# Performance work log

Hardware: AMD Instinct MI355X
Metric: run time of the kernel (lower is better)

The kernel has to match this reference:

```python
import jax, jax.numpy as jnp
import numpy as np

B, DEPTH, X, H, C = 512, 9, 128, 64, 16
NPT = 2 ** (DEPTH + 1) - 1  # 1023 nodes per perfect binary tree (heap layout)


def setup_inputs() -> dict:
    key = jax.random.key(0)
    ks = jax.random.split(key, 5)
    s = 0.05
    return {
        "embeddings": jax.random.normal(ks[0], (B, NPT, X), jnp.float32),
        "h0": jnp.zeros((B, NPT, H), jnp.float32),
        "c0": jnp.zeros((B, NPT, H), jnp.float32),
        "W_iou": jax.random.normal(ks[1], (X, 3 * H), jnp.float32) * s,
        "U_iou": jax.random.normal(ks[2], (2 * H, 3 * H), jnp.float32) * s,
        "b_iou": jnp.zeros((3 * H,), jnp.float32),
        "Uf_w": jax.random.normal(ks[3], (2 * H, 2 * H), jnp.float32) * s,
        "Uf_b": jnp.zeros((2 * H,), jnp.float32),
        "lin_w": jax.random.normal(ks[4], (H, C), jnp.float32) * s,
        "lin_b": jnp.zeros((C,), jnp.float32),
    }


def _apply_gates(iou, c_base):
    # apply_node_func: i,o,u chunks -> c = sig(i)*tanh(u) + c_base; h = sig(o)*tanh(c)
    i, o, u = jnp.split(iou, 3, axis=-1)
    c = jax.nn.sigmoid(i) * jnp.tanh(u) + c_base
    h = jax.nn.sigmoid(o) * jnp.tanh(c)
    return h, c


def reference(embeddings, h0, c0, W_iou, U_iou, b_iou, Uf_w, Uf_b, lin_w, lin_b):
    h, c = h0, c0
    # --- leaves (no in-edges): iou = W_iou(x) + b_iou, c_base = initial c ---
    ls = 2 ** DEPTH - 1  # first leaf index
    iou = embeddings[:, ls:] @ W_iou + b_iou
    hl, cl = _apply_gates(iou, c0[:, ls:])
    h = h.at[:, ls:].set(hl)
    c = c.at[:, ls:].set(cl)
    # --- internal levels, deepest -> root (topological propagation) ---
    for lvl in range(DEPTH - 1, -1, -1):
        s0, n = 2 ** lvl - 1, 2 ** lvl
        # children of nodes [s0, s0+n) are the contiguous block [2*s0+1, 2*s0+1+2n)
        cs = 2 * s0 + 1
        hc = h[:, cs:cs + 2 * n].reshape(B, n, 2 * H)   # h_cat = [h_left, h_right]
        cc = c[:, cs:cs + 2 * n].reshape(B, n, 2, H)
        # reduce_func: f = sigmoid(U_f(h_cat)); c_red = sum(f * c_children)
        f = jax.nn.sigmoid(hc @ Uf_w.T + Uf_b).reshape(B, n, 2, H)
        c_red = jnp.sum(f * cc, axis=2)
        # DGL overwrite semantics: internal iou = U_iou(h_cat) (+ b_iou in apply)
        iou = hc @ U_iou + b_iou
        hn, cn = _apply_gates(iou, c_red)
        h = h.at[:, s0:s0 + n].set(hn)
        c = c.at[:, s0:s0 + n].set(cn)
    # global mean pool over nodes per tree, then classifier + softmax
    hm = jnp.mean(h, axis=1)  # [B, H]
    logits = hm @ lin_w + lin_b
    return jax.nn.softmax(logits, axis=-1)
```

## Files before the change

### kernel.cpp

```cpp
#include <hip/hip_runtime.h>
#include <hip/hip_bf16.h>
#include <stdint.h>

#define NPT 1023
#define LEAF_TILES 12
#define INT_TILES  20

typedef float f32x4 __attribute__((ext_vector_type(4)));
typedef __bf16 bf16x8_t __attribute__((ext_vector_type(8)));

__device__ __forceinline__ unsigned int f32_to_bf16(float f) {
    unsigned int u = __float_as_uint(f);
    u += 0x7FFFu + ((u >> 16) & 1u);
    return u >> 16;
}
__device__ __forceinline__ float sigm(float x) {
    return __builtin_amdgcn_rcpf(1.0f + __expf(-x));
}
__device__ __forceinline__ float tanh_f(float x) {
    return 1.0f - 2.0f * __builtin_amdgcn_rcpf(1.0f + __expf(2.0f * x));
}
__device__ __forceinline__ f32x4 mfma16(uint4 a, uint4 b, f32x4 c) {
    return __builtin_amdgcn_mfma_f32_16x16x32_bf16(
        __builtin_bit_cast(bf16x8_t, a), __builtin_bit_cast(bf16x8_t, b), c, 0, 0, 0);
}

__global__ void prep_kernel(const float* __restrict__ W_iou,
                            const float* __restrict__ U_iou,
                            const float* __restrict__ Uf_w,
                            unsigned short* __restrict__ leafB,
                            unsigned short* __restrict__ intB) {
    int tid = blockIdx.x * blockDim.x + threadIdx.x;
    const int leaf_slots = LEAF_TILES * 4 * 64;
    const int total = (LEAF_TILES + INT_TILES) * 4 * 64;
    if (tid >= total) return;
    bool leaf = tid < leaf_slots;
    int s = leaf ? tid : tid - leaf_slots;
    int tile = s >> 8;
    int ks = (s >> 6) & 3;
    int l = s & 63;
    int col = tile * 16 + (l & 15);
    int k0 = ks * 32 + (l >> 4) * 8;
    unsigned short vals[8];
#pragma unroll
    for (int i = 0; i < 8; ++i) {
        int k = k0 + i;
        float v;
        if (leaf) v = W_iou[k * 192 + col];
        else      v = (col < 192) ? U_iou[k * 192 + col]
                                  : Uf_w[(col - 192) * 128 + k];
        vals[i] = (unsigned short)f32_to_bf16(v);
    }
    uint4* dst = (uint4*)(leaf ? leafB : intB);
    dst[s] = *(const uint4*)vals;
}

__global__ __launch_bounds__(256, 2) void mega_kernel(
        const float* __restrict__ emb,
        float* __restrict__ hbuf,
        float* __restrict__ cbuf,
        const unsigned short* __restrict__ leafB,
        const unsigned short* __restrict__ intB,
        const float* __restrict__ b_iou,
        const float* __restrict__ Uf_b) {
    __shared__ unsigned char cEven[32768];
    __shared__ unsigned char cOdd[16384];
    __shared__ unsigned char hB[16384];

    const int tid = threadIdx.x;
    const int t = blockIdx.x >> 2, e = blockIdx.x & 3;
    const int wave = tid >> 6, lane = tid & 63;
    const int lrow = lane & 15, kgrp = lane >> 4;
    const int c = wave * 16 + lrow;

    const uint4* BfL = (const uint4*)leafB;
    uint4 BL[12];
#pragma unroll
    for (int nt = 0; nt < 3; ++nt)
#pragma unroll
        for (int ks = 0; ks < 4; ++ks)
            BL[nt * 4 + ks] = BfL[((wave + 4 * nt) * 4 + ks) * 64 + lane];

    const float* embBase = emb + ((size_t)(t * NPT + 511 + 128 * e)) * 128;
#pragma unroll
    for (int it = 0; it < 8; ++it) {
        int qid = it * 256 + tid;
        int r = qid >> 4, j = qid & 15;
        const float* s = embBase + r * 128 + j * 8;
        float4 v0 = *(const float4*)s;
        float4 v1 = *(const float4*)(s + 4);
        uint4 pk;
        pk.x = f32_to_bf16(v0.x) | (f32_to_bf16(v0.y) << 16);
        pk.y = f32_to_bf16(v0.z) | (f32_to_bf16(v0.w) << 16);
        pk.z = f32_to_bf16(v1.x) | (f32_to_bf16(v1.y) << 16);
        pk.w = f32_to_bf16(v1.z) | (f32_to_bf16(v1.w) << 16);
        *(uint4*)&cEven[r * 256 + ((j ^ (r & 15)) << 4)] = pk;
    }
    __syncthreads();

    f32x4 acc[8][3];
#pragma unroll
    for (int mt = 0; mt < 8; ++mt)
#pragma unroll
        for (int nt = 0; nt < 3; ++nt)
            acc[mt][nt] = (f32x4){0.f, 0.f, 0.f, 0.f};
#pragma unroll
    for (int mt = 0; mt < 8; ++mt) {
        const int row = mt * 16 + lrow;
        uint4 A[4];
#pragma unroll
        for (int ks = 0; ks < 4; ++ks)
            A[ks] = *(const uint4*)&cEven[row * 256 + (((4 * ks + kgrp) ^ (row & 15)) << 4)];
#pragma unroll
        for (int nt = 0; nt < 3; ++nt)
#pragma unroll
            for (int ks = 0; ks < 4; ++ks)
                acc[mt][nt] = mfma16(A[ks], BL[nt * 4 + ks], acc[mt][nt]);
    }
    __syncthreads();

    const float bi = b_iou[c], bo = b_iou[64 + c], bu = b_iou[128 + c];
    const float bfl = Uf_b[c], bfr = Uf_b[64 + c];
    float psum = 0.f;

#pragma unroll
    for (int mt = 0; mt < 8; ++mt)
#pragma unroll
        for (int q = 0; q < 4; ++q) {
            const int row = mt * 16 + kgrp * 4 + q;
            float i_ = acc[mt][0][q] + bi;
            float o_ = acc[mt][1][q] + bo;
            float u_ = acc[mt][2][q] + bu;
            float cn = sigm(i_) * tanh_f(u_);
            float hn = sigm(o_) * tanh_f(cn);
            psum += hn;
            *(float*)&cEven[(row * 64 + c) * 4] = cn;
            *(unsigned short*)&hB[row * 128 + (((c >> 3) ^ ((row >> 1) & 7)) << 4) + (c & 7) * 2] =
                (unsigned short)f32_to_bf16(hn);
        }

    const uint4* BfI = (const uint4*)intB;
    uint4 BI[20];
#pragma unroll
    for (int nt = 0; nt < 5; ++nt)
#pragma unroll
        for (int ks = 0; ks < 4; ++ks)
            BI[nt * 4 + ks] = BfI[((wave + 4 * nt) * 4 + ks) * 64 + lane];
    __syncthreads();

    for (int lvl = 1; lvl <= 7; ++lvl) {
        const int M = 128 >> lvl;
        const int MT = (M + 15) >> 4;
        f32x4 acc2[4][5];
#pragma unroll
        for (int mt = 0; mt < 4; ++mt)
#pragma unroll
            for (int nt = 0; nt < 5; ++nt)
                acc2[mt][nt] = (f32x4){0.f, 0.f, 0.f, 0.f};
#pragma unroll
        for (int mt = 0; mt < 4; ++mt) if (mt < MT) {
            const int row = mt * 16 + lrow;
            uint4 A[4];
#pragma unroll
            for (int ks = 0; ks < 4; ++ks) {
                const int n = 2 * row + (ks >> 1);
                A[ks] = *(const uint4*)&hB[n * 128 + ((((ks & 1) * 4 + kgrp) ^ (row & 7)) << 4)];
            }
#pragma unroll
            for (int nt = 0; nt < 5; ++nt)
#pragma unroll
                for (int ks = 0; ks < 4; ++ks)
                    acc2[mt][nt] = mfma16(A[ks], BI[nt * 4 + ks], acc2[mt][nt]);
        }
        __syncthreads();
        const float* cChild = (const float*)((lvl & 1) ? cEven : cOdd);
        float* cPar = (float*)((lvl & 1) ? cOdd : cEven);
#pragma unroll
        for (int mt = 0; mt < 4; ++mt) if (mt < MT)
#pragma unroll
            for (int q = 0; q < 4; ++q) {
                const int row = mt * 16 + kgrp * 4 + q;
                if (row < M) {
                    float cl = cChild[(2 * row) * 64 + c];
                    float cr = cChild[(2 * row + 1) * 64 + c];
                    float i_ = acc2[mt][0][q] + bi;
                    float o_ = acc2[mt][1][q] + bo;
                    float u_ = acc2[mt][2][q] + bu;
                    float fl = sigm(acc2[mt][3][q] + bfl);
                    float fr = sigm(acc2[mt][4][q] + bfr);
                    float cn = sigm(i_) * tanh_f(u_) + fl * cl + fr * cr;
                    float hn = sigm(o_) * tanh_f(cn);
                    psum += hn;
                    if (lvl < 7) {
                        cPar[row * 64 + c] = cn;
                        *(unsigned short*)&hB[row * 128 + (((c >> 3) ^ ((row >> 1) & 7)) << 4) + (c & 7) * 2] =
                            (unsigned short)f32_to_bf16(hn);
                    } else {
                        size_t gi = ((size_t)(t * NPT + 3 + e)) * 64 + c;
                        hbuf[gi] = hn;
                        cbuf[gi] = cn;
                    }
                }
            }
        __syncthreads();
    }

    psum += __shfl_xor(psum, 16);
    psum += __shfl_xor(psum, 32);
    if (kgrp == 0)
        hbuf[((size_t)(t * NPT + 8 + e)) * 64 + c] = psum;
}

__global__ __launch_bounds__(256) void final_kernel(
        float* __restrict__ hbuf,
        const float* __restrict__ cbuf,
        const unsigned short* __restrict__ intB,
        const float* __restrict__ b_iou,
        const float* __restrict__ Uf_b,
        const float* __restrict__ lin_w,
        const float* __restrict__ lin_b,
        float* __restrict__ out) {
    __shared__ unsigned short hc1[16][128];
    __shared__ unsigned short hc0[16][128];
    __shared__ float sc[4][64];
    __shared__ float c12[2][64];
    __shared__ float hm[64];

    const int tid = threadIdx.x;
    const int t = blockIdx.x;
    const int wave = tid >> 6, lane = tid & 63;
    const int lrow = lane & 15, kgrp = lane >> 4;
    const int c = wave * 16 + lrow;

    {
        const int nd = tid >> 6, col = tid & 63;
        size_t gi = ((size_t)(t * NPT + 3 + nd)) * 64 + col;
        float hv = hbuf[gi];
        sc[nd][col] = cbuf[gi];
        hc1[nd >> 1][(nd & 1) * 64 + col] = (unsigned short)f32_to_bf16(hv);
    }
    const uint4* BfI = (const uint4*)intB;
    uint4 BI[20];
#pragma unroll
    for (int nt = 0; nt < 5; ++nt)
#pragma unroll
        for (int ks = 0; ks < 4; ++ks)
            BI[nt * 4 + ks] = BfI[((wave + 4 * nt) * 4 + ks) * 64 + lane];
    __syncthreads();

    const float bi = b_iou[c], bo = b_iou[64 + c], bu = b_iou[128 + c];
    const float bfl = Uf_b[c], bfr = Uf_b[64 + c];
    float psum = 0.f;

    f32x4 a1[5];
#pragma unroll
    for (int nt = 0; nt < 5; ++nt) a1[nt] = (f32x4){0.f, 0.f, 0.f, 0.f};
#pragma unroll
    for (int ks = 0; ks < 4; ++ks) {
        uint4 A = *(const uint4*)&hc1[lrow][ks * 32 + kgrp * 8];
#pragma unroll
        for (int nt = 0; nt < 5; ++nt) a1[nt] = mfma16(A, BI[nt * 4 + ks], a1[nt]);
    }
#pragma unroll
    for (int q = 0; q < 4; ++q) {
        const int row = kgrp * 4 + q;
        if (row < 2) {
            float cl = sc[2 * row][c];
            float cr = sc[2 * row + 1][c];
            float i_ = a1[0][q] + bi, o_ = a1[1][q] + bo, u_ = a1[2][q] + bu;
            float fl = sigm(a1[3][q] + bfl), fr = sigm(a1[4][q] + bfr);
            float cn = sigm(i_) * tanh_f(u_) + fl * cl + fr * cr;
            float hn = sigm(o_) * tanh_f(cn);
            psum += hn;
            c12[row][c] = cn;
            hc0[0][row * 64 + c] = (unsigned short)f32_to_bf16(hn);
        }
    }
    __syncthreads();

    f32x4 a0[5];
#pragma unroll
    for (int nt = 0; nt < 5; ++nt) a0[nt] = (f32x4){0.f, 0.f, 0.f, 0.f};
#pragma unroll
    for (int ks = 0; ks < 4; ++ks) {
        uint4 A = *(const uint4*)&hc0[lrow][ks * 32 + kgrp * 8];
#pragma unroll
        for (int nt = 0; nt < 5; ++nt) a0[nt] = mfma16(A, BI[nt * 4 + ks], a0[nt]);
    }
    if (kgrp == 0) {
        float cl = c12[0][c], cr = c12[1][c];
        float i_ = a0[0][0] + bi, o_ = a0[1][0] + bo, u_ = a0[2][0] + bu;
        float fl = sigm(a0[3][0] + bfl), fr = sigm(a0[4][0] + bfr);
        float cn = sigm(i_) * tanh_f(u_) + fl * cl + fr * cr;
        float hn = sigm(o_) * tanh_f(cn);
        psum += hn;
    }

    psum += __shfl_xor(psum, 16);
    psum += __shfl_xor(psum, 32);
    if (kgrp == 0) hm[c] = psum;
    __syncthreads();
    if (tid < 64) {
        float s = hm[tid];
#pragma unroll
        for (int e2 = 0; e2 < 4; ++e2)
            s += hbuf[((size_t)(t * NPT + 8 + e2)) * 64 + tid];
        hm[tid] = s * (1.0f / 1023.0f);
    }
    __syncthreads();
    if (tid < 16) {
        int cc = tid;
        float lg = lin_b[cc];
#pragma unroll
        for (int dd = 0; dd < 64; ++dd) lg += hm[dd] * lin_w[dd * 16 + cc];
        float mx = lg;
#pragma unroll
        for (int off = 8; off; off >>= 1) mx = fmaxf(mx, __shfl_xor(mx, off, 16));
        float ex = expf(lg - mx);
        float sm = ex;
#pragma unroll
        for (int off = 8; off; off >>= 1) sm += __shfl_xor(sm, off, 16);
        out[t * 16 + cc] = ex / sm;
    }
}

extern "C" void kernel_launch(void* const* d_in, const int* in_sizes, int n_in,
                              void* d_out, int out_size, void* d_ws, size_t ws_size,
                              hipStream_t stream) {
    const float* emb   = (const float*)d_in[0];
    float*       hbuf  = (float*)d_in[1];
    float*       cbuf  = (float*)d_in[2];
    const float* W_iou = (const float*)d_in[3];
    const float* U_iou = (const float*)d_in[4];
    const float* b_iou = (const float*)d_in[5];
    const float* Uf_w  = (const float*)d_in[6];
    const float* Uf_b  = (const float*)d_in[7];
    const float* lin_w = (const float*)d_in[8];
    const float* lin_b = (const float*)d_in[9];
    float* out = (float*)d_out;

    unsigned short* leafB = (unsigned short*)d_ws;
    unsigned short* intB  = leafB + (size_t)LEAF_TILES * 4 * 64 * 8;

    prep_kernel<<<32, 256, 0, stream>>>(W_iou, U_iou, Uf_w, leafB, intB);
    mega_kernel<<<2048, 256, 0, stream>>>(emb, hbuf, cbuf, leafB, intB, b_iou, Uf_b);
    final_kernel<<<512, 256, 0, stream>>>(hbuf, cbuf, intB, b_iou, Uf_b, lin_w, lin_b, out);
}
```

Baseline: 493.3 us.

## Cut LDS and register use to fit three blocks per CU

```diff
diff --git a/kernel.cpp b/kernel.cpp
--- a/kernel.cpp
+++ b/kernel.cpp
@@ -13,6 +13,9 @@
     unsigned int u = __float_as_uint(f);
     u += 0x7FFFu + ((u >> 16) & 1u);
     return u >> 16;
+}
+__device__ __forceinline__ float bf16_ld(const void* p) {
+    return __uint_as_float(((unsigned int)*(const unsigned short*)p) << 16);
 }
 __device__ __forceinline__ float sigm(float x) {
     return __builtin_amdgcn_rcpf(1.0f + __expf(-x));
@@ -55,7 +58,7 @@
     dst[s] = *(const uint4*)vals;
 }
 
-__global__ __launch_bounds__(256, 2) void mega_kernel(
+__global__ __launch_bounds__(256, 3) void mega_kernel(
         const float* __restrict__ emb,
         float* __restrict__ hbuf,
         float* __restrict__ cbuf,
@@ -63,9 +66,8 @@
         const unsigned short* __restrict__ intB,
         const float* __restrict__ b_iou,
         const float* __restrict__ Uf_b) {
-    __shared__ unsigned char cEven[32768];
-    __shared__ unsigned char cOdd[16384];
-    __shared__ unsigned char hB[16384];
+    __shared__ __align__(16) unsigned char cw[32768];
+    __shared__ __align__(16) unsigned char hB[16384];
 
     const int tid = threadIdx.x;
     const int t = blockIdx.x >> 2, e = blockIdx.x & 3;
@@ -94,28 +96,7 @@
         pk.y = f32_to_bf16(v0.z) | (f32_to_bf16(v0.w) << 16);
         pk.z = f32_to_bf16(v1.x) | (f32_to_bf16(v1.y) << 16);
         pk.w = f32_to_bf16(v1.z) | (f32_to_bf16(v1.w) << 16);
-        *(uint4*)&cEven[r * 256 + ((j ^ (r & 15)) << 4)] = pk;
-    }
-    __syncthreads();
-
-    f32x4 acc[8][3];
-#pragma unroll
-    for (int mt = 0; mt < 8; ++mt)
-#pragma unroll
-        for (int nt = 0; nt < 3; ++nt)
-            acc[mt][nt] = (f32x4){0.f, 0.f, 0.f, 0.f};
-#pragma unroll
-    for (int mt = 0; mt < 8; ++mt) {
-        const int row = mt * 16 + lrow;
-        uint4 A[4];
-#pragma unroll
-        for (int ks = 0; ks < 4; ++ks)
-            A[ks] = *(const uint4*)&cEven[row * 256 + (((4 * ks + kgrp) ^ (row & 15)) << 4)];
-#pragma unroll
-        for (int nt = 0; nt < 3; ++nt)
-#pragma unroll
-            for (int ks = 0; ks < 4; ++ks)
-                acc[mt][nt] = mfma16(A[ks], BL[nt * 4 + ks], acc[mt][nt]);
+        *(uint4*)&cw[r * 256 + ((j ^ (r & 15)) << 4)] = pk;
     }
     __syncthreads();
 
@@ -124,20 +105,43 @@
     float psum = 0.f;
 
 #pragma unroll
-    for (int mt = 0; mt < 8; ++mt)
-#pragma unroll
-        for (int q = 0; q < 4; ++q) {
-            const int row = mt * 16 + kgrp * 4 + q;
-            float i_ = acc[mt][0][q] + bi;
-            float o_ = acc[mt][1][q] + bo;
-            float u_ = acc[mt][2][q] + bu;
-            float cn = sigm(i_) * tanh_f(u_);
-            float hn = sigm(o_) * tanh_f(cn);
-            psum += hn;
-            *(float*)&cEven[(row * 64 + c) * 4] = cn;
-            *(unsigned short*)&hB[row * 128 + (((c >> 3) ^ ((row >> 1) & 7)) << 4) + (c & 7) * 2] =
-                (unsigned short)f32_to_bf16(hn);
+    for (int p = 0; p < 2; ++p) {
+        f32x4 acc[4][3];
+#pragma unroll
+        for (int mt = 0; mt < 4; ++mt)
+#pragma unroll
+            for (int nt = 0; nt < 3; ++nt)
+                acc[mt][nt] = (f32x4){0.f, 0.f, 0.f, 0.f};
+#pragma unroll
+        for (int mt = 0; mt < 4; ++mt) {
+            const int row = p * 64 + mt * 16 + lrow;
+            uint4 A[4];
+#pragma unroll
+            for (int ks = 0; ks < 4; ++ks)
+                A[ks] = *(const uint4*)&cw[row * 256 + (((4 * ks + kgrp) ^ (row & 15)) << 4)];
+#pragma unroll
+            for (int nt = 0; nt < 3; ++nt)
+#pragma unroll
+                for (int ks = 0; ks < 4; ++ks)
+                    acc[mt][nt] = mfma16(A[ks], BL[nt * 4 + ks], acc[mt][nt]);
         }
+        if (p == 0) __syncthreads();
+#pragma unroll
+        for (int mt = 0; mt < 4; ++mt)
+#pragma unroll
+            for (int q = 0; q < 4; ++q) {
+                const int row = p * 64 + mt * 16 + kgrp * 4 + q;
+                float i_ = acc[mt][0][q] + bi;
+                float o_ = acc[mt][1][q] + bo;
+                float u_ = acc[mt][2][q] + bu;
+                float cn = sigm(i_) * tanh_f(u_);
+                float hn = sigm(o_) * tanh_f(cn);
+                psum += hn;
+                *(unsigned short*)&cw[(row * 64 + c) * 2] = (unsigned short)f32_to_bf16(cn);
+                *(unsigned short*)&hB[row * 128 + (((c >> 3) ^ ((row >> 1) & 7)) << 4) + (c & 7) * 2] =
+                    (unsigned short)f32_to_bf16(hn);
+            }
+    }
 
     const uint4* BfI = (const uint4*)intB;
     uint4 BI[20];
@@ -148,17 +152,64 @@
             BI[nt * 4 + ks] = BfI[((wave + 4 * nt) * 4 + ks) * 64 + lane];
     __syncthreads();
 
-    for (int lvl = 1; lvl <= 7; ++lvl) {
+#pragma unroll
+    for (int p = 0; p < 2; ++p) {
+        f32x4 acc2[2][5];
+#pragma unroll
+        for (int mt = 0; mt < 2; ++mt)
+#pragma unroll
+            for (int nt = 0; nt < 5; ++nt)
+                acc2[mt][nt] = (f32x4){0.f, 0.f, 0.f, 0.f};
+#pragma unroll
+        for (int mt = 0; mt < 2; ++mt) {
+            const int row = p * 32 + mt * 16 + lrow;
+            uint4 A[4];
+#pragma unroll
+            for (int ks = 0; ks < 4; ++ks) {
+                const int n = 2 * row + (ks >> 1);
+                A[ks] = *(const uint4*)&hB[n * 128 + ((((ks & 1) * 4 + kgrp) ^ (row & 7)) << 4)];
+            }
+#pragma unroll
+            for (int nt = 0; nt < 5; ++nt)
+#pragma unroll
+                for (int ks = 0; ks < 4; ++ks)
+                    acc2[mt][nt] = mfma16(A[ks], BI[nt * 4 + ks], acc2[mt][nt]);
+        }
+        if (p == 0) __syncthreads();
+        float* cPar = (float*)(cw + 16384);
+#pragma unroll
+        for (int mt = 0; mt < 2; ++mt)
+#pragma unroll
+            for (int q = 0; q < 4; ++q) {
+                const int row = p * 32 + mt * 16 + kgrp * 4 + q;
+                float cl = bf16_ld(&cw[((2 * row) * 64 + c) * 2]);
+                float cr = bf16_ld(&cw[((2 * row + 1) * 64 + c) * 2]);
+                float i_ = acc2[mt][0][q] + bi;
+                float o_ = acc2[mt][1][q] + bo;
+                float u_ = acc2[mt][2][q] + bu;
+                float fl = sigm(acc2[mt][3][q] + bfl);
+                float fr = sigm(acc2[mt][4][q] + bfr);
+                float cn = sigm(i_) * tanh_f(u_) + fl * cl + fr * cr;
+                float hn = sigm(o_) * tanh_f(cn);
+                psum += hn;
+                cPar[row * 64 + c] = cn;
+                *(unsigned short*)&hB[row * 128 + (((c >> 3) ^ ((row >> 1) & 7)) << 4) + (c & 7) * 2] =
+                    (unsigned short)f32_to_bf16(hn);
+            }
+    }
+    __syncthreads();
+
+    for (int lvl = 2; lvl <= 7; ++lvl) {
         const int M = 128 >> lvl;
         const int MT = (M + 15) >> 4;
-        f32x4 acc2[4][5];
-#pragma unroll
-        for (int mt = 0; mt < 4; ++mt)
+        f32x4 acc2[2][5];
+#pragma unroll
+        for (int mt = 0; mt < 2; ++mt)
 #pragma unroll
             for (int nt = 0; nt < 5; ++nt)
                 acc2[mt][nt] = (f32x4){0.f, 0.f, 0.f, 0.f};
 #pragma unroll
-        for (int mt = 0; mt < 4; ++mt) if (mt < MT) {
+        for (int mt = 0; mt < 2; ++mt) if (mt < MT) {
             const int row = mt * 16 + lrow;
             uint4 A[4];
 #pragma unroll
@@ -173,10 +224,10 @@
                     acc2[mt][nt] = mfma16(A[ks], BI[nt * 4 + ks], acc2[mt][nt]);
         }
         __syncthreads();
-        const float* cChild = (const float*)((lvl & 1) ? cEven : cOdd);
-        float* cPar = (float*)((lvl & 1) ? cOdd : cEven);
-#pragma unroll
-        for (int mt = 0; mt < 4; ++mt) if (mt < MT)
+        const float* cChild = (const float*)(cw + ((lvl & 1) ? 0 : 16384));
+        float* cPar = (float*)(cw + ((lvl & 1) ? 16384 : 0));
+#pragma unroll
+        for (int mt = 0; mt < 2; ++mt) if (mt < MT)
 #pragma unroll
             for (int q = 0; q < 4; ++q) {
                 const int row = mt * 16 + kgrp * 4 + q;
```

Measured after the change: 507.7 us. 1.03x slower.
